# Kernel optimization log

Measured on AMD Instinct MI355X. Metric: run time of the kernel, lower is better.

The kernel has to match this reference:

```python
import jax, jax.numpy as jnp
import numpy as np

B, N, K = 4, 8192, 16
EMBED, HID, NCLS = 64, 128, 13
EPS = 1e-5


def _bn(x, g, b):
    # BatchNorm1d in training mode: stats over all points (B*N), per channel
    m = jnp.mean(x, axis=(0, 1), keepdims=True)
    v = jnp.var(x, axis=(0, 1), keepdims=True)
    return (x - m) * jax.lax.rsqrt(v + EPS) * g + b


def _knn_idx(pos, k):
    # pos: [B,N,3] -> k nearest neighbor indices per point (self excluded)
    sq = jnp.sum(pos * pos, -1)  # [B,N]
    d2 = sq[:, :, None] + sq[:, None, :] - 2.0 * jnp.einsum('bnd,bmd->bnm', pos, pos)
    n = pos.shape[1]
    d2 = d2 + jnp.eye(n, dtype=pos.dtype) * 1e10  # mask self (loop=False)
    _, idx = jax.lax.top_k(-d2, k)  # [B,N,k]
    return idx


def _pt_conv(x, pos, idx, w_lin, w_src, w_dst, pos_w, pos_b):
    # PyG PointTransformerConv: vector attention over neighbors (incl. self loop)
    Bc = x.shape[0]
    bidx = jnp.arange(Bc)[:, None, None]
    v = x @ w_lin          # value:  lin(x)
    a_src = x @ w_src      # lin_src(x)
    a_dst = x @ w_dst      # lin_dst(x)
    vj = v[bidx, idx]                      # [B,N,k1,C]
    aj = a_src[bidx, idx]                  # [B,N,k1,C]
    pj = pos[bidx, idx]                    # [B,N,k1,3]
    delta = (pos[:, :, None, :] - pj) @ pos_w + pos_b   # pos_nn(pos_i - pos_j)
    attn = jax.nn.softmax(a_dst[:, :, None, :] - aj + delta, axis=2)
    return jnp.sum(attn * (vj + delta), axis=2)  # sum aggregation


def setup_inputs() -> dict:
    key = jax.random.key(0)
    ks = jax.random.split(key, 20)

    def w(k, fan_in, fan_out):
        return (jax.random.normal(k, (fan_in, fan_out), jnp.float32) / np.sqrt(fan_in)).astype(jnp.float32)

    inp = {
        'points': jax.random.normal(ks[0], (B, N, 3), jnp.float32),
        'embed_w1': w(ks[1], 3, EMBED), 'embed_b1': jnp.zeros((EMBED,), jnp.float32),
        'bn1_g': jnp.ones((EMBED,), jnp.float32), 'bn1_b': jnp.zeros((EMBED,), jnp.float32),
        'embed_w2': w(ks[2], EMBED, EMBED), 'embed_b2': jnp.zeros((EMBED,), jnp.float32),
        'bne_g': jnp.ones((EMBED,), jnp.float32), 'bne_b': jnp.zeros((EMBED,), jnp.float32),
        'l0_lin': w(ks[3], EMBED, HID), 'l0_src': w(ks[4], EMBED, HID), 'l0_dst': w(ks[5], EMBED, HID),
        'l0_pos_w': w(ks[6], 3, HID), 'l0_pos_b': jnp.zeros((HID,), jnp.float32),
        'l0_bn_g': jnp.ones((HID,), jnp.float32), 'l0_bn_b': jnp.zeros((HID,), jnp.float32),
        'l1_lin': w(ks[7], HID, HID), 'l1_src': w(ks[8], HID, HID), 'l1_dst': w(ks[9], HID, HID),
        'l1_pos_w': w(ks[10], 3, HID), 'l1_pos_b': jnp.zeros((HID,), jnp.float32),
        'l1_bn_g': jnp.ones((HID,), jnp.float32), 'l1_bn_b': jnp.zeros((HID,), jnp.float32),
        'dec_w1': w(ks[11], HID, HID), 'dec_b1': jnp.zeros((HID,), jnp.float32),
        'dec_bn_g': jnp.ones((HID,), jnp.float32), 'dec_bn_b': jnp.zeros((HID,), jnp.float32),
        'dec_w2': w(ks[12], HID, NCLS), 'dec_b2': jnp.zeros((NCLS,), jnp.float32),
    }
    return inp


def reference(points, embed_w1, embed_b1, bn1_g, bn1_b, embed_w2, embed_b2,
              bne_g, bne_b,
              l0_lin, l0_src, l0_dst, l0_pos_w, l0_pos_b, l0_bn_g, l0_bn_b,
              l1_lin, l1_src, l1_dst, l1_pos_w, l1_pos_b, l1_bn_g, l1_bn_b,
              dec_w1, dec_b1, dec_bn_g, dec_bn_b, dec_w2, dec_b2):
    Bc, Nc, _ = points.shape
    # embedding MLP: Linear -> BN -> ReLU -> Linear, then BN -> ReLU
    h = points @ embed_w1 + embed_b1
    h = jax.nn.relu(_bn(h, bn1_g, bn1_b))
    h = h @ embed_w2 + embed_b2
    x = jax.nn.relu(_bn(h, bne_g, bne_b))
    # kNN graph (per batch), then append self loop (add_self_loops=True)
    idx = _knn_idx(points, K)
    self_idx = jnp.broadcast_to(jnp.arange(Nc)[None, :, None], (Bc, Nc, 1))
    idxf = jnp.concatenate([idx, self_idx], axis=-1)  # [B,N,K+1]
    x = jax.nn.relu(_bn(_pt_conv(x, points, idxf, l0_lin, l0_src, l0_dst, l0_pos_w, l0_pos_b), l0_bn_g, l0_bn_b))
    x = jax.nn.relu(_bn(_pt_conv(x, points, idxf, l1_lin, l1_src, l1_dst, l1_pos_w, l1_pos_b), l1_bn_g, l1_bn_b))
    # decoder MLP (dropout = identity at inference)
    h = jax.nn.relu(_bn(x @ dec_w1 + dec_b1, dec_bn_g, dec_bn_b))
    logits = h @ dec_w2 + dec_b2  # [B,N,num_classes]
    return logits
```

## Files before the change

### kernel.cpp

```cpp
#include <hip/hip_runtime.h>
#include <math.h>

#define BB 4
#define NN 8192
#define PP 32768
#define KNN 16

typedef float f32x2 __attribute__((ext_vector_type(2)));
typedef float f32x4 __attribute__((ext_vector_type(4)));

__device__ __forceinline__ f32x2 pk_mul(f32x2 a, f32x2 b) {
  f32x2 d; asm("v_pk_mul_f32 %0, %1, %2" : "=v"(d) : "v"(a), "v"(b)); return d;
}
__device__ __forceinline__ f32x2 pk_add(f32x2 a, f32x2 b) {
  f32x2 d; asm("v_pk_add_f32 %0, %1, %2" : "=v"(d) : "v"(a), "v"(b)); return d;
}

__global__ __launch_bounds__(256) void k_embed1(const float* __restrict__ pts,
    const float* __restrict__ w1, const float* __restrict__ b1, float* __restrict__ h1)
{
  int tid = threadIdx.x;
  int c = tid & 63, g = tid >> 6;
  float wx = w1[c], wy = w1[64 + c], wz = w1[128 + c], bc = b1[c];
  int base = blockIdx.x * 256;
  #pragma unroll 4
  for (int i = 0; i < 64; ++i) {
    int p = base + g + i * 4;
    float px = pts[p*3+0], py = pts[p*3+1], pz = pts[p*3+2];
    float h = fmaf(pz, wz, fmaf(py, wy, fmaf(px, wx, bc)));
    h1[(size_t)p*64 + c] = h;
  }
}

__global__ __launch_bounds__(256) void k_prep(const float* __restrict__ pts, float* __restrict__ pp)
{
  int t = blockIdx.x * 256 + threadIdx.x;
  int b = t >> 12, m = t & 4095;
  int c = m >> 4, l = m & 15;
  int jl = b * NN + c * 32 + l;
  int jh = jl + 16;
  float xl = pts[jl*3+0], yl = pts[jl*3+1], zl = pts[jl*3+2];
  float xh = pts[jh*3+0], yh = pts[jh*3+1], zh = pts[jh*3+2];
  float wl = __fadd_rn(__fadd_rn(__fmul_rn(xl,xl), __fmul_rn(yl,yl)), __fmul_rn(zl,zl));
  float wh = __fadd_rn(__fadd_rn(__fmul_rn(xh,xh), __fmul_rn(yh,yh)), __fmul_rn(zh,zh));
  float* o = pp + (size_t)t * 8;
  *(float4*)(o + 0) = make_float4(xl, xh, yl, yh);
  *(float4*)(o + 4) = make_float4(zl, zh, wl, wh);
}

template<int C>
__global__ __launch_bounds__(256) void k_stats(const float* __restrict__ src,
    float* __restrict__ gsum, float* __restrict__ gss)
{
  constexpr int GPB = 256 / C;
  int tid = threadIdx.x;
  int c = tid % C, g = tid / C;
  float s = 0.f, ss = 0.f;
  for (int p = blockIdx.x * GPB + g; p < PP; p += gridDim.x * GPB) {
    float v = src[(size_t)p*C + c];
    s += v; ss = fmaf(v, v, ss);
  }
  __shared__ float ls[256], lq[256];
  ls[tid] = s; lq[tid] = ss;
  __syncthreads();
  if (tid < C) {
    float a = 0.f, b2 = 0.f;
    #pragma unroll
    for (int i = 0; i < GPB; ++i) { a += ls[tid + i*C]; b2 += lq[tid + i*C]; }
    atomicAdd(gsum + tid, a);
    atomicAdd(gss + tid, b2);
  }
}

__global__ void k_finalize(int C, const float* __restrict__ gsum, const float* __restrict__ gss,
    const float* __restrict__ gg, const float* __restrict__ bb,
    float* __restrict__ sc, float* __restrict__ sh)
{
  int c = threadIdx.x;
  if (c >= C) return;
  float mean = gsum[c] * (1.0f / PP);
  float var  = gss[c] * (1.0f / PP) - mean * mean;
  float s = gg[c] / sqrtf(var + 1e-5f);
  sc[c] = s;
  sh[c] = bb[c] - mean * s;
}

template<int K, int COUT>
__global__ __launch_bounds__(256) void k_proj(const float* __restrict__ in,
    const float* __restrict__ sc, const float* __restrict__ sh,
    const float* __restrict__ W0, const float* __restrict__ W1, const float* __restrict__ W2,
    const float* __restrict__ B0, const float* __restrict__ B1, const float* __restrict__ B2,
    float* __restrict__ O0, float* __restrict__ O1, float* __restrict__ O2)
{
  constexpr int PTS = 64;
  constexpr int CW = 8;
  constexpr int CG = COUT / CW;
  constexpr int PW = PTS * CG / 256;
  const float* W  = (blockIdx.y == 0) ? W0 : (blockIdx.y == 1) ? W1 : W2;
  const float* Bb = (blockIdx.y == 0) ? B0 : (blockIdx.y == 1) ? B1 : B2;
  float*       O  = (blockIdx.y == 0) ? O0 : (blockIdx.y == 1) ? O1 : O2;
  __shared__ float xs[PTS][K + 1];
  int tid = threadIdx.x;
  int pbase = blockIdx.x * PTS;
  constexpr int T4 = PTS * K / 4;
  for (int i = tid; i < T4; i += 256) {
    int p = i / (K/4), k = (i % (K/4)) * 4;
    float4 v = *(const float4*)(in + (size_t)(pbase + p)*K + k);
    v.x = fmaxf(fmaf(v.x, sc[k+0], sh[k+0]), 0.f);
    v.y = fmaxf(fmaf(v.y, sc[k+1], sh[k+1]), 0.f);
    v.z = fmaxf(fmaf(v.z, sc[k+2], sh[k+2]), 0.f);
    v.w = fmaxf(fmaf(v.w, sc[k+3], sh[k+3]), 0.f);
    xs[p][k+0] = v.x; xs[p][k+1] = v.y; xs[p][k+2] = v.z; xs[p][k+3] = v.w;
  }
  __syncthreads();
  int cg = tid % CG, pg = tid / CG;
  int c0 = cg * CW, p0 = pg * PW;
  float acc[PW][CW];
  #pragma unroll
  for (int i = 0; i < PW; ++i) {
    #pragma unroll
    for (int j = 0; j < CW; ++j) acc[i][j] = 0.f;
  }
  #pragma unroll 4
  for (int k = 0; k < K; ++k) {
    float4 wa = *(const float4*)(W + (size_t)k*COUT + c0);
    float4 wb = *(const float4*)(W + (size_t)k*COUT + c0 + 4);
    #pragma unroll
    for (int i = 0; i < PW; ++i) {
      float x = xs[p0 + i][k];
      acc[i][0] = fmaf(x, wa.x, acc[i][0]);
      acc[i][1] = fmaf(x, wa.y, acc[i][1]);
      acc[i][2] = fmaf(x, wa.z, acc[i][2]);
      acc[i][3] = fmaf(x, wa.w, acc[i][3]);
      acc[i][4] = fmaf(x, wb.x, acc[i][4]);
      acc[i][5] = fmaf(x, wb.y, acc[i][5]);
      acc[i][6] = fmaf(x, wb.z, acc[i][6]);
      acc[i][7] = fmaf(x, wb.w, acc[i][7]);
    }
  }
  float bj[CW];
  #pragma unroll
  for (int j = 0; j < CW; ++j) bj[j] = Bb ? Bb[c0 + j] : 0.f;
  #pragma unroll
  for (int i = 0; i < PW; ++i) {
    float* op = O + (size_t)(pbase + p0 + i)*COUT + c0;
    *(float4*)(op)     = make_float4(acc[i][0]+bj[0], acc[i][1]+bj[1], acc[i][2]+bj[2], acc[i][3]+bj[3]);
    *(float4*)(op + 4) = make_float4(acc[i][4]+bj[4], acc[i][5]+bj[5], acc[i][6]+bj[6], acc[i][7]+bj[7]);
  }
}

__global__ __launch_bounds__(256, 8) void k_knn(const float* __restrict__ pp, int* __restrict__ idxout)
{
  int tid = threadIdx.x;
  int lane = tid & 63;
  int l16 = lane & 15;
  int g64 = lane & 48;
  int wv = (blockIdx.x * 256 + tid) >> 6;
  int b  = wv >> 11;
  int qbase = (wv * 4) & (NN - 1);
  int qc = qbase >> 5;
  int qr = (qbase & 31) + (lane >> 4);
  const float* pb = pp + (size_t)b * (NN * 4);

  float qx, qy, qz, qw;
  {
    int qslot = qc * 16 + (qr & 15);
    int qh = (qr >> 4) & 1;
    const float* qp = pb + (size_t)qslot * 8 + qh;
    qx = qp[0]; qy = qp[2]; qz = qp[4]; qw = qp[6];
  }
  f32x2 qx2; qx2.x = qx; qx2.y = qx;
  f32x2 qy2; qy2.x = qy; qy2.y = qy;
  f32x2 qz2; qz2.x = qz; qz2.y = qz;
  f32x2 qw2; qw2.x = qw; qw2.y = qw;

  int addr_push = (lane + 1) << 2;
  int addr_tau  = (g64 + 15) << 2;

  float lval = 3.4e38f;
  int   lidx = 0;
  float tau  = 3.4e38f;

  auto half_pass = [&](float d2, int jbase) {
    unsigned long long bal = __ballot(d2 < tau);
    if (bal) {
      unsigned slice = (unsigned)(bal >> g64) & 0xffffu;
      while (__ballot(slice != 0)) {
        bool live = slice != 0;
        int src = __ffs((int)slice) - 1;
        slice &= slice - 1;
        int ab = (g64 + (src & 15)) << 2;
        float v = __uint_as_float(__builtin_amdgcn_ds_bpermute(ab, __float_as_uint(d2)));
        if (!live) v = 3.4e38f;
        int jc = jbase + src;
        float pv = __uint_as_float(__builtin_amdgcn_ds_permute(addr_push, __float_as_uint(lval)));
        int   pi = __builtin_amdgcn_ds_permute(addr_push, lidx);
        bool atpos = (l16 == 0) || (pv <= v);
        if (lval > v) {
          lval = atpos ? v  : pv;
          lidx = atpos ? jc : pi;
        }
      }
      tau = __uint_as_float(__builtin_amdgcn_ds_bpermute(addr_tau, __float_as_uint(lval)));
    }
  };

  const float* cp = pb + (size_t)l16 * 8;

  {
    f32x4 A  = *(const f32x4*)(cp + 0);
    f32x4 Bq = *(const f32x4*)(cp + 4);
    cp += 128;
    f32x2 xs = __builtin_shufflevector(A, A, 0, 1);
    f32x2 ys = __builtin_shufflevector(A, A, 2, 3);
    f32x2 zs = __builtin_shufflevector(Bq, Bq, 0, 1);
    f32x2 ws = __builtin_shufflevector(Bq, Bq, 2, 3);
    f32x2 dot = pk_add(pk_add(pk_mul(qx2, xs), pk_mul(qy2, ys)), pk_mul(qz2, zs));
    f32x2 s2  = pk_add(qw2, ws);
    f32x2 t2  = pk_add(dot, dot);
    float d2lo = __fsub_rn(s2.x, t2.x);
    float d2hi = __fsub_rn(s2.y, t2.y);
    if (qc == 0) {
      bool lo = qr < 16;
      int  tl = lo ? qr : qr - 16;
      if (l16 == tl) { if (lo) d2lo = 3.4e38f; else d2hi = 3.4e38f; }
    }
    float v = d2lo; int ix = l16;
    #pragma unroll
    for (int k = 2; k <= 16; k <<= 1) {
      #pragma unroll
      for (int j = k >> 1; j >= 1; j >>= 1) {
        float ov = __shfl_xor(v, j, 16);
        int   oi = __shfl_xor(ix, j, 16);
        bool up    = (l16 & k) == 0;
        bool lower = (l16 & j) == 0;
        bool lt = (ov < v) || (ov == v && oi < ix);
        if ((up == lower) ? lt : !lt) { v = ov; ix = oi; }
      }
    }
    lval = v; lidx = ix;
    tau = __uint_as_float(__builtin_amdgcn_ds_bpermute(addr_tau, __float_as_uint(lval)));
    half_pass(d2hi, 16);
  }

  for (int c = 1; c < 256; ++c) {
    f32x4 A  = *(const f32x4*)(cp + 0);
    f32x4 Bq = *(const f32x4*)(cp + 4);
    cp += 128;
    f32x2 xs = __builtin_shufflevector(A, A, 0, 1);
    f32x2 ys = __builtin_shufflevector(A, A, 2, 3);
    f32x2 zs = __builtin_shufflevector(Bq, Bq, 0, 1);
    f32x2 ws = __builtin_shufflevector(Bq, Bq, 2, 3);
    f32x2 dot = pk_add(pk_add(pk_mul(qx2, xs), pk_mul(qy2, ys)), pk_mul(qz2, zs));
    f32x2 s2  = pk_add(qw2, ws);
    f32x2 t2  = pk_add(dot, dot);
    float d2lo = __fsub_rn(s2.x, t2.x);
    float d2hi = __fsub_rn(s2.y, t2.y);
    if (c == qc) {
      bool lo = qr < 16;
      int  tl = lo ? qr : qr - 16;
      if (l16 == tl) { if (lo) d2lo = 3.4e38f; else d2hi = 3.4e38f; }
    }
    half_pass(d2lo, c * 32);
    half_pass(d2hi, c * 32 + 16);
  }

  idxout[(size_t)wv * 64 + lane] = lidx;
}

__global__ __launch_bounds__(256) void k_conv(const float* __restrict__ V, const float* __restrict__ S,
    const float* __restrict__ D, const float* __restrict__ pts, const int* __restrict__ idx,
    const float* __restrict__ pw, const float* __restrict__ pbv, float* __restrict__ Y)
{
  int lane = threadIdx.x & 63;
  int wid  = (blockIdx.x * 256 + threadIdx.x) >> 6;
  int c0 = lane * 2;
  float2 w0  = *(const float2*)(pw + c0);
  float2 w1  = *(const float2*)(pw + 128 + c0);
  float2 w2  = *(const float2*)(pw + 256 + c0);
  float2 pb2 = *(const float2*)(pbv + c0);
  for (int p = wid; p < PP; p += 4096) {
    int b = p >> 13, self = p & (NN - 1);
    const float* pbase = pts + (size_t)b * NN * 3;
    float pix = pbase[self*3+0], piy = pbase[self*3+1], piz = pbase[self*3+2];
    float2 di = *(const float2*)(D + (size_t)p*128 + c0);
    float m0 = -3.4e38f, m1 = -3.4e38f, l0 = 0.f, l1 = 0.f, a0 = 0.f, a1 = 0.f;
    for (int t = 0; t < 17; ++t) {
      int j = (t < 16) ? idx[p*KNN + t] : self;
      float dx = pix - pbase[j*3+0];
      float dy = piy - pbase[j*3+1];
      float dz = piz - pbase[j*3+2];
      size_t off = ((size_t)b * NN + j) * 128 + c0;
      float2 sj = *(const float2*)(S + off);
      float2 vj = *(const float2*)(V + off);
      float de0 = fmaf(dz, w2.x, fmaf(dy, w1.x, fmaf(dx, w0.x, pb2.x)));
      float de1 = fmaf(dz, w2.y, fmaf(dy, w1.y, fmaf(dx, w0.y, pb2.y)));
      float g0 = di.x - sj.x + de0;
      float g1 = di.y - sj.y + de1;
      float mn0 = fmaxf(m0, g0), mn1 = fmaxf(m1, g1);
      float cr0 = __expf(m0 - mn0), cr1 = __expf(m1 - mn1);
      float e0  = __expf(g0 - mn0), e1  = __expf(g1 - mn1);
      l0 = fmaf(l0, cr0, e0);
      l1 = fmaf(l1, cr1, e1);
      a0 = fmaf(a0, cr0, e0 * (vj.x + de0));
      a1 = fmaf(a1, cr1, e1 * (vj.y + de1));
      m0 = mn0; m1 = mn1;
    }
    float2 o; o.x = a0 / l0; o.y = a1 / l1;
    *(float2*)(Y + (size_t)p*128 + c0) = o;
  }
}

__global__ __launch_bounds__(256) void k_dec2(const float* __restrict__ T,
    const float* __restrict__ sc, const float* __restrict__ sh,
    const float* __restrict__ W, const float* __restrict__ bias, float* __restrict__ out)
{
  __shared__ float xs[64][132];
  __shared__ float wt[13][128];
  int tid = threadIdx.x;
  int pb = blockIdx.x * 64;
  for (int i = tid; i < 13 * 128; i += 256) {
    int cls = i >> 7, k = i & 127;
    wt[cls][k] = W[k*13 + cls];
  }
  for (int i = tid; i < 64 * 32; i += 256) {
    int p = i >> 5, k = (i & 31) * 4;
    float4 v = *(const float4*)(T + (size_t)(pb + p)*128 + k);
    v.x = fmaxf(fmaf(v.x, sc[k+0], sh[k+0]), 0.f);
    v.y = fmaxf(fmaf(v.y, sc[k+1], sh[k+1]), 0.f);
    v.z = fmaxf(fmaf(v.z, sc[k+2], sh[k+2]), 0.f);
    v.w = fmaxf(fmaf(v.w, sc[k+3], sh[k+3]), 0.f);
    xs[p][k+0] = v.x; xs[p][k+1] = v.y; xs[p][k+2] = v.z; xs[p][k+3] = v.w;
  }
  __syncthreads();
  for (int o = tid; o < 64 * 13; o += 256) {
    int p = o / 13, cls = o - p * 13;
    float acc = bias[cls];
    const float4* xr = (const float4*)&xs[p][0];
    const float4* wr = (const float4*)&wt[cls][0];
    #pragma unroll 8
    for (int k4 = 0; k4 < 32; ++k4) {
      float4 a = xr[k4], w = wr[k4];
      acc = fmaf(a.x, w.x, acc);
      acc = fmaf(a.y, w.y, acc);
      acc = fmaf(a.z, w.z, acc);
      acc = fmaf(a.w, w.w, acc);
    }
    out[(size_t)(pb + p)*13 + cls] = acc;
  }
}

extern "C" void kernel_launch(void* const* d_in, const int* in_sizes, int n_in,
                              void* d_out, int out_size, void* d_ws, size_t ws_size,
                              hipStream_t stream)
{
  const float* pts      = (const float*)d_in[0];
  const float* embed_w1 = (const float*)d_in[1];
  const float* embed_b1 = (const float*)d_in[2];
  const float* bn1_g    = (const float*)d_in[3];
  const float* bn1_b    = (const float*)d_in[4];
  const float* embed_w2 = (const float*)d_in[5];
  const float* embed_b2 = (const float*)d_in[6];
  const float* bne_g    = (const float*)d_in[7];
  const float* bne_b    = (const float*)d_in[8];
  const float* l0_lin   = (const float*)d_in[9];
  const float* l0_src   = (const float*)d_in[10];
  const float* l0_dst   = (const float*)d_in[11];
  const float* l0_pos_w = (const float*)d_in[12];
  const float* l0_pos_b = (const float*)d_in[13];
  const float* l0_bn_g  = (const float*)d_in[14];
  const float* l0_bn_b  = (const float*)d_in[15];
  const float* l1_lin   = (const float*)d_in[16];
  const float* l1_src   = (const float*)d_in[17];
  const float* l1_dst   = (const float*)d_in[18];
  const float* l1_pos_w = (const float*)d_in[19];
  const float* l1_pos_b = (const float*)d_in[20];
  const float* l1_bn_g  = (const float*)d_in[21];
  const float* l1_bn_b  = (const float*)d_in[22];
  const float* dec_w1   = (const float*)d_in[23];
  const float* dec_b1   = (const float*)d_in[24];
  const float* dec_bn_g = (const float*)d_in[25];
  const float* dec_bn_b = (const float*)d_in[26];
  const float* dec_w2   = (const float*)d_in[27];
  const float* dec_b2   = (const float*)d_in[28];

  char* ws = (char*)d_ws;
  const size_t MB = 1024 * 1024;
  float* h1  = (float*)(ws + 0);
  float* h2  = (float*)(ws + 8*MB);
  int*   idx = (int*)  (ws + 16*MB);
  float* v0  = (float*)(ws + 18*MB);
  float* s0  = (float*)(ws + 34*MB);
  float* d0  = (float*)(ws + 50*MB);
  float* y0  = (float*)(ws + 66*MB);
  float* y1  = (float*)(ws + 82*MB);
  float* tt  = (float*)(ws + 0);
  float* pairs8 = (float*)(ws + 18*MB);
  float* st  = (float*)(ws + 98*MB);
  float *sum1=st+0,    *ss1=st+64,   *sc1=st+128,  *sh1=st+192;
  float *sum2=st+256,  *ss2=st+320,  *sc2=st+384,  *sh2=st+448;
  float *sum3=st+512,  *ss3=st+640,  *sc3=st+768,  *sh3=st+896;
  float *sum4=st+1024, *ss4=st+1152, *sc4=st+1280, *sh4=st+1408;
  float *sum5=st+1536, *ss5=st+1664, *sc5=st+1792, *sh5=st+1920;

  hipMemsetAsync(st, 0, 2048 * sizeof(float), stream);

  k_prep<<<64, 256, 0, stream>>>(pts, pairs8);
  k_knn<<<2048, 256, 0, stream>>>(pairs8, idx);

  k_embed1<<<128, 256, 0, stream>>>(pts, embed_w1, embed_b1, h1);
  k_stats<64><<<512, 256, 0, stream>>>(h1, sum1, ss1);
  k_finalize<<<1, 64, 0, stream>>>(64, sum1, ss1, bn1_g, bn1_b, sc1, sh1);
  k_proj<64,64><<<dim3(512,1), 256, 0, stream>>>(h1, sc1, sh1,
      embed_w2, embed_w2, embed_w2, embed_b2, embed_b2, embed_b2, h2, h2, h2);
  k_stats<64><<<512, 256, 0, stream>>>(h2, sum2, ss2);
  k_finalize<<<1, 64, 0, stream>>>(64, sum2, ss2, bne_g, bne_b, sc2, sh2);

  k_proj<64,128><<<dim3(512,3), 256, 0, stream>>>(h2, sc2, sh2,
      l0_lin, l0_src, l0_dst, nullptr, nullptr, nullptr, v0, s0, d0);
  k_conv<<<1024, 256, 0, stream>>>(v0, s0, d0, pts, idx, l0_pos_w, l0_pos_b, y0);
  k_stats<128><<<512, 256, 0, stream>>>(y0, sum3, ss3);
  k_finalize<<<1, 128, 0, stream>>>(128, sum3, ss3, l0_bn_g, l0_bn_b, sc3, sh3);

  k_proj<128,128><<<dim3(512,3), 256, 0, stream>>>(y0, sc3, sh3,
      l1_lin, l1_src, l1_dst, nullptr, nullptr, nullptr, v0, s0, d0);
  k_conv<<<1024, 256, 0, stream>>>(v0, s0, d0, pts, idx, l1_pos_w, l1_pos_b, y1);
  k_stats<128><<<512, 256, 0, stream>>>(y1, sum4, ss4);
  k_finalize<<<1, 128, 0, stream>>>(128, sum4, ss4, l1_bn_g, l1_bn_b, sc4, sh4);

  k_proj<128,128><<<dim3(512,1), 256, 0, stream>>>(y1, sc4, sh4,
      dec_w1, dec_w1, dec_w1, dec_b1, dec_b1, dec_b1, tt, tt, tt);
  k_stats<128><<<512, 256, 0, stream>>>(tt, sum5, ss5);
  k_finalize<<<1, 128, 0, stream>>>(128, sum5, ss5, dec_bn_g, dec_bn_b, sc5, sh5);
  k_dec2<<<512, 256, 0, stream>>>(tt, sc5, sh5, dec_w2, dec_b2, (float*)d_out);
}
```

Before: 689.7 us.

## Buffer kNN candidates in LDS and merge via bitonic sort on flush

Replaces the per-candidate serial insertion into the lane-distributed top-16 list with a pending buffer. Candidates that beat the threshold are compacted into shared memory using ballot/popcount. When the buffer would overflow, the 16 pending candidates are bitonic-sorted and merged with the current list. This amortises the serial permute-based insertion loop over batches of up to 16 hits, at the cost of extra LDS traffic and a tau that is refreshed less often.

```diff
diff --git a/kernel.cpp b/kernel.cpp
--- a/kernel.cpp
+++ b/kernel.cpp
@@ -5,6 +5,8 @@
 #define NN 8192
 #define PP 32768
 #define KNN 16
+#define KINF 3.4e38f
+#define PADIDX 0x7fffffff
 
 typedef float f32x2 __attribute__((ext_vector_type(2)));
 typedef float f32x4 __attribute__((ext_vector_type(4)));
@@ -151,10 +153,12 @@
 
 __global__ __launch_bounds__(256, 8) void k_knn(const float* __restrict__ pp, int* __restrict__ idxout)
 {
+  __shared__ uint2 buf[256];
   int tid = threadIdx.x;
   int lane = tid & 63;
   int l16 = lane & 15;
   int g64 = lane & 48;
+  uint2* wbuf = buf + (tid >> 6) * 64;
   int wv = (blockIdx.x * 256 + tid) >> 6;
   int b  = wv >> 11;
   int qbase = (wv * 4) & (NN - 1);
@@ -174,76 +178,60 @@
   f32x2 qz2; qz2.x = qz; qz2.y = qz;
   f32x2 qw2; qw2.x = qw; qw2.y = qw;
 
-  int addr_push = (lane + 1) << 2;
-  int addr_tau  = (g64 + 15) << 2;
-
-  float lval = 3.4e38f;
-  int   lidx = 0;
-  float tau  = 3.4e38f;
-
-  auto half_pass = [&](float d2, int jbase) {
-    unsigned long long bal = __ballot(d2 < tau);
-    if (bal) {
-      unsigned slice = (unsigned)(bal >> g64) & 0xffffu;
-      while (__ballot(slice != 0)) {
-        bool live = slice != 0;
-        int src = __ffs((int)slice) - 1;
-        slice &= slice - 1;
-        int ab = (g64 + (src & 15)) << 2;
-        float v = __uint_as_float(__builtin_amdgcn_ds_bpermute(ab, __float_as_uint(d2)));
-        if (!live) v = 3.4e38f;
-        int jc = jbase + src;
-        float pv = __uint_as_float(__builtin_amdgcn_ds_permute(addr_push, __float_as_uint(lval)));
-        int   pi = __builtin_amdgcn_ds_permute(addr_push, lidx);
-        bool atpos = (l16 == 0) || (pv <= v);
-        if (lval > v) {
-          lval = atpos ? v  : pv;
-          lidx = atpos ? jc : pi;
-        }
-      }
-      tau = __uint_as_float(__builtin_amdgcn_ds_bpermute(addr_tau, __float_as_uint(lval)));
-    }
-  };
-
-  const float* cp = pb + (size_t)l16 * 8;
-
-  {
-    f32x4 A  = *(const f32x4*)(cp + 0);
-    f32x4 Bq = *(const f32x4*)(cp + 4);
-    cp += 128;
-    f32x2 xs = __builtin_shufflevector(A, A, 0, 1);
-    f32x2 ys = __builtin_shufflevector(A, A, 2, 3);
-    f32x2 zs = __builtin_shufflevector(Bq, Bq, 0, 1);
-    f32x2 ws = __builtin_shufflevector(Bq, Bq, 2, 3);
-    f32x2 dot = pk_add(pk_add(pk_mul(qx2, xs), pk_mul(qy2, ys)), pk_mul(qz2, zs));
-    f32x2 s2  = pk_add(qw2, ws);
-    f32x2 t2  = pk_add(dot, dot);
-    float d2lo = __fsub_rn(s2.x, t2.x);
-    float d2hi = __fsub_rn(s2.y, t2.y);
-    if (qc == 0) {
-      bool lo = qr < 16;
-      int  tl = lo ? qr : qr - 16;
-      if (l16 == tl) { if (lo) d2lo = 3.4e38f; else d2hi = 3.4e38f; }
-    }
-    float v = d2lo; int ix = l16;
+  float lval = KINF; int lidx = PADIDX;
+  float pval = KINF; int pidx = PADIDX;
+  int   pcnt = 0;
+  float tau  = KINF;
+  unsigned lmask = (1u << l16) - 1;
+
+  auto flush = [&]() {
+    float v = (l16 >= pcnt) ? KINF : pval;
+    int  ix = (l16 >= pcnt) ? PADIDX : pidx;
     #pragma unroll
     for (int k = 2; k <= 16; k <<= 1) {
       #pragma unroll
-      for (int j = k >> 1; j >= 1; j >>= 1) {
-        float ov = __shfl_xor(v, j, 16);
-        int   oi = __shfl_xor(ix, j, 16);
-        bool up    = (l16 & k) == 0;
-        bool lower = (l16 & j) == 0;
-        bool lt = (ov < v) || (ov == v && oi < ix);
-        if ((up == lower) ? lt : !lt) { v = ov; ix = oi; }
+      for (int m = k >> 1; m >= 1; m >>= 1) {
+        float ov = __shfl_xor(v, m, 16);
+        int   oi = __shfl_xor(ix, m, 16);
+        bool dirUp = (l16 & k) == 0;
+        bool lower = (l16 & m) == 0;
+        bool oLt = (ov < v) || (ov == v && oi < ix);
+        if ((dirUp == lower) ? oLt : !oLt) { v = ov; ix = oi; }
       }
     }
-    lval = v; lidx = ix;
-    tau = __uint_as_float(__builtin_amdgcn_ds_bpermute(addr_tau, __float_as_uint(lval)));
-    half_pass(d2hi, 16);
-  }
-
-  for (int c = 1; c < 256; ++c) {
+    float rv = __shfl_xor(v, 15, 16);
+    int   ri = __shfl_xor(ix, 15, 16);
+    bool t = (rv < lval) || (rv == lval && ri < lidx);
+    float nv = t ? rv : lval;
+    int   ni = t ? ri : lidx;
+    #pragma unroll
+    for (int m = 8; m >= 1; m >>= 1) {
+      float ov = __shfl_xor(nv, m, 16);
+      int   oi = __shfl_xor(ni, m, 16);
+      bool lower = (l16 & m) == 0;
+      bool oLt = (ov < nv) || (ov == nv && oi < ni);
+      if (lower ? oLt : !oLt) { nv = ov; ni = oi; }
+    }
+    lval = nv; lidx = ni;
+    tau = __shfl(lval, 15, 16);
+    pcnt = 0;
+  };
+
+  auto append = [&](unsigned long long bal, bool hit, float d2, int j) {
+    unsigned slice = (unsigned)(bal >> g64) & 0xffffu;
+    int h   = __popc(slice);
+    int pos = __popc(slice & lmask);
+    if (__ballot(pcnt + h > 16)) flush();
+    if (hit) wbuf[g64 + pcnt + pos] = make_uint2(__float_as_uint(d2), (unsigned)j);
+    uint2 r = wbuf[lane];
+    bool targ = (l16 >= pcnt) && (l16 < pcnt + h);
+    pval = targ ? __uint_as_float(r.x) : pval;
+    pidx = targ ? (int)r.y : pidx;
+    pcnt += h;
+  };
+
+  const float* cp = pb + (size_t)l16 * 8;
+  for (int c = 0; c < 256; ++c) {
     f32x4 A  = *(const f32x4*)(cp + 0);
     f32x4 Bq = *(const f32x4*)(cp + 4);
     cp += 128;
@@ -259,11 +247,16 @@
     if (c == qc) {
       bool lo = qr < 16;
       int  tl = lo ? qr : qr - 16;
-      if (l16 == tl) { if (lo) d2lo = 3.4e38f; else d2hi = 3.4e38f; }
-    }
-    half_pass(d2lo, c * 32);
-    half_pass(d2hi, c * 32 + 16);
-  }
+      if (l16 == tl) { if (lo) d2lo = KINF; else d2hi = KINF; }
+    }
+    bool hlo = d2lo < tau;
+    unsigned long long blo = __ballot(hlo);
+    if (blo) append(blo, hlo, d2lo, c * 32 + l16);
+    bool hhi = d2hi < tau;
+    unsigned long long bhi = __ballot(hhi);
+    if (bhi) append(bhi, hhi, d2hi, c * 32 + 16 + l16);
+  }
+  flush();
 
   idxout[(size_t)wv * 64 + lane] = lidx;
 }
```

Result: no change. 698.9 us (+1.3%).

## Fuse BatchNorm statistics into producer kernels and finalize inside consumers

Applied to the files above, without the earlier changes.

Per-channel sum and sum-of-squares accumulation moves into the epilogues of embed1, proj and conv, so the separate k_stats passes no longer re-read each activation tensor. The finalize step (mean, variance, scale, shift) is now computed per block inside the consuming proj and dec2 kernels, which removes five tiny k_finalize launches. The cost is extra shuffles, shared-memory reductions and atomics in each producer, plus a few redundant rsqrt computations per block.

```diff
diff --git a/kernel.cpp b/kernel.cpp
--- a/kernel.cpp
+++ b/kernel.cpp
@@ -17,18 +17,30 @@
 }
 
 __global__ __launch_bounds__(256) void k_embed1(const float* __restrict__ pts,
-    const float* __restrict__ w1, const float* __restrict__ b1, float* __restrict__ h1)
+    const float* __restrict__ w1, const float* __restrict__ b1, float* __restrict__ h1,
+    float* __restrict__ gsum, float* __restrict__ gss)
 {
   int tid = threadIdx.x;
   int c = tid & 63, g = tid >> 6;
   float wx = w1[c], wy = w1[64 + c], wz = w1[128 + c], bc = b1[c];
   int base = blockIdx.x * 256;
+  float s = 0.f, ss = 0.f;
   #pragma unroll 4
   for (int i = 0; i < 64; ++i) {
     int p = base + g + i * 4;
     float px = pts[p*3+0], py = pts[p*3+1], pz = pts[p*3+2];
     float h = fmaf(pz, wz, fmaf(py, wy, fmaf(px, wx, bc)));
     h1[(size_t)p*64 + c] = h;
+    s += h; ss = fmaf(h, h, ss);
+  }
+  __shared__ float ls[256], lq[256];
+  ls[tid] = s; lq[tid] = ss;
+  __syncthreads();
+  if (tid < 64) {
+    float a  = ls[tid] + ls[tid+64] + ls[tid+128] + ls[tid+192];
+    float b2 = lq[tid] + lq[tid+64] + lq[tid+128] + lq[tid+192];
+    atomicAdd(gsum + tid, a);
+    atomicAdd(gss  + tid, b2);
   }
 }
 
@@ -48,49 +60,14 @@
   *(float4*)(o + 4) = make_float4(zl, zh, wl, wh);
 }
 
-template<int C>
-__global__ __launch_bounds__(256) void k_stats(const float* __restrict__ src,
-    float* __restrict__ gsum, float* __restrict__ gss)
-{
-  constexpr int GPB = 256 / C;
-  int tid = threadIdx.x;
-  int c = tid % C, g = tid / C;
-  float s = 0.f, ss = 0.f;
-  for (int p = blockIdx.x * GPB + g; p < PP; p += gridDim.x * GPB) {
-    float v = src[(size_t)p*C + c];
-    s += v; ss = fmaf(v, v, ss);
-  }
-  __shared__ float ls[256], lq[256];
-  ls[tid] = s; lq[tid] = ss;
-  __syncthreads();
-  if (tid < C) {
-    float a = 0.f, b2 = 0.f;
-    #pragma unroll
-    for (int i = 0; i < GPB; ++i) { a += ls[tid + i*C]; b2 += lq[tid + i*C]; }
-    atomicAdd(gsum + tid, a);
-    atomicAdd(gss + tid, b2);
-  }
-}
-
-__global__ void k_finalize(int C, const float* __restrict__ gsum, const float* __restrict__ gss,
-    const float* __restrict__ gg, const float* __restrict__ bb,
-    float* __restrict__ sc, float* __restrict__ sh)
-{
-  int c = threadIdx.x;
-  if (c >= C) return;
-  float mean = gsum[c] * (1.0f / PP);
-  float var  = gss[c] * (1.0f / PP) - mean * mean;
-  float s = gg[c] / sqrtf(var + 1e-5f);
-  sc[c] = s;
-  sh[c] = bb[c] - mean * s;
-}
-
-template<int K, int COUT>
+template<int K, int COUT, bool STATS>
 __global__ __launch_bounds__(256) void k_proj(const float* __restrict__ in,
-    const float* __restrict__ sc, const float* __restrict__ sh,
+    const float* __restrict__ gsumI, const float* __restrict__ gssI,
+    const float* __restrict__ gamma, const float* __restrict__ beta,
     const float* __restrict__ W0, const float* __restrict__ W1, const float* __restrict__ W2,
     const float* __restrict__ B0, const float* __restrict__ B1, const float* __restrict__ B2,
-    float* __restrict__ O0, float* __restrict__ O1, float* __restrict__ O2)
+    float* __restrict__ O0, float* __restrict__ O1, float* __restrict__ O2,
+    float* __restrict__ gsumO, float* __restrict__ gssO)
 {
   constexpr int PTS = 64;
   constexpr int CW = 8;
@@ -100,16 +77,25 @@
   const float* Bb = (blockIdx.y == 0) ? B0 : (blockIdx.y == 1) ? B1 : B2;
   float*       O  = (blockIdx.y == 0) ? O0 : (blockIdx.y == 1) ? O1 : O2;
   __shared__ float xs[PTS][K + 1];
+  __shared__ float scs[K], shs[K];
   int tid = threadIdx.x;
+  if (tid < K) {
+    float mean = gsumI[tid] * (1.0f / PP);
+    float var  = gssI[tid] * (1.0f / PP) - mean * mean;
+    float s = gamma[tid] / sqrtf(var + 1e-5f);
+    scs[tid] = s;
+    shs[tid] = beta[tid] - mean * s;
+  }
+  __syncthreads();
   int pbase = blockIdx.x * PTS;
   constexpr int T4 = PTS * K / 4;
   for (int i = tid; i < T4; i += 256) {
     int p = i / (K/4), k = (i % (K/4)) * 4;
     float4 v = *(const float4*)(in + (size_t)(pbase + p)*K + k);
-    v.x = fmaxf(fmaf(v.x, sc[k+0], sh[k+0]), 0.f);
-    v.y = fmaxf(fmaf(v.y, sc[k+1], sh[k+1]), 0.f);
-    v.z = fmaxf(fmaf(v.z, sc[k+2], sh[k+2]), 0.f);
-    v.w = fmaxf(fmaf(v.w, sc[k+3], sh[k+3]), 0.f);
+    v.x = fmaxf(fmaf(v.x, scs[k+0], shs[k+0]), 0.f);
+    v.y = fmaxf(fmaf(v.y, scs[k+1], shs[k+1]), 0.f);
+    v.z = fmaxf(fmaf(v.z, scs[k+2], shs[k+2]), 0.f);
+    v.w = fmaxf(fmaf(v.w, scs[k+3], shs[k+3]), 0.f);
     xs[p][k+0] = v.x; xs[p][k+1] = v.y; xs[p][k+2] = v.z; xs[p][k+3] = v.w;
   }
   __syncthreads();
@@ -141,11 +127,44 @@
   float bj[CW];
   #pragma unroll
   for (int j = 0; j < CW; ++j) bj[j] = Bb ? Bb[c0 + j] : 0.f;
+  float sj[CW], qj[CW];
+  #pragma unroll
+  for (int j = 0; j < CW; ++j) { sj[j] = 0.f; qj[j] = 0.f; }
   #pragma unroll
   for (int i = 0; i < PW; ++i) {
     float* op = O + (size_t)(pbase + p0 + i)*COUT + c0;
-    *(float4*)(op)     = make_float4(acc[i][0]+bj[0], acc[i][1]+bj[1], acc[i][2]+bj[2], acc[i][3]+bj[3]);
-    *(float4*)(op + 4) = make_float4(acc[i][4]+bj[4], acc[i][5]+bj[5], acc[i][6]+bj[6], acc[i][7]+bj[7]);
+    float o0 = acc[i][0]+bj[0], o1 = acc[i][1]+bj[1], o2 = acc[i][2]+bj[2], o3 = acc[i][3]+bj[3];
+    float o4 = acc[i][4]+bj[4], o5 = acc[i][5]+bj[5], o6 = acc[i][6]+bj[6], o7 = acc[i][7]+bj[7];
+    *(float4*)(op)     = make_float4(o0, o1, o2, o3);
+    *(float4*)(op + 4) = make_float4(o4, o5, o6, o7);
+    if (STATS) {
+      sj[0]+=o0; sj[1]+=o1; sj[2]+=o2; sj[3]+=o3; sj[4]+=o4; sj[5]+=o5; sj[6]+=o6; sj[7]+=o7;
+      qj[0]=fmaf(o0,o0,qj[0]); qj[1]=fmaf(o1,o1,qj[1]); qj[2]=fmaf(o2,o2,qj[2]); qj[3]=fmaf(o3,o3,qj[3]);
+      qj[4]=fmaf(o4,o4,qj[4]); qj[5]=fmaf(o5,o5,qj[5]); qj[6]=fmaf(o6,o6,qj[6]); qj[7]=fmaf(o7,o7,qj[7]);
+    }
+  }
+  if (STATS) {
+    #pragma unroll
+    for (int off = CG; off < 64; off <<= 1) {
+      #pragma unroll
+      for (int j = 0; j < CW; ++j) {
+        sj[j] += __shfl_xor(sj[j], off);
+        qj[j] += __shfl_xor(qj[j], off);
+      }
+    }
+    __shared__ float ws[4][COUT], wq[4][COUT];
+    int wid = tid >> 6, lane = tid & 63;
+    if (lane < CG) {
+      #pragma unroll
+      for (int j = 0; j < CW; ++j) { ws[wid][lane*CW+j] = sj[j]; wq[wid][lane*CW+j] = qj[j]; }
+    }
+    __syncthreads();
+    if (tid < COUT) {
+      float a  = ws[0][tid] + ws[1][tid] + ws[2][tid] + ws[3][tid];
+      float b2 = wq[0][tid] + wq[1][tid] + wq[2][tid] + wq[3][tid];
+      atomicAdd(gsumO + tid, a);
+      atomicAdd(gssO  + tid, b2);
+    }
   }
 }
 
@@ -270,15 +289,18 @@
 
 __global__ __launch_bounds__(256) void k_conv(const float* __restrict__ V, const float* __restrict__ S,
     const float* __restrict__ D, const float* __restrict__ pts, const int* __restrict__ idx,
-    const float* __restrict__ pw, const float* __restrict__ pbv, float* __restrict__ Y)
-{
-  int lane = threadIdx.x & 63;
-  int wid  = (blockIdx.x * 256 + threadIdx.x) >> 6;
+    const float* __restrict__ pw, const float* __restrict__ pbv, float* __restrict__ Y,
+    float* __restrict__ gsum, float* __restrict__ gss)
+{
+  int tid = threadIdx.x;
+  int lane = tid & 63;
+  int wid  = (blockIdx.x * 256 + tid) >> 6;
   int c0 = lane * 2;
   float2 w0  = *(const float2*)(pw + c0);
   float2 w1  = *(const float2*)(pw + 128 + c0);
   float2 w2  = *(const float2*)(pw + 256 + c0);
   float2 pb2 = *(const float2*)(pbv + c0);
+  float st0 = 0.f, st1 = 0.f, sq0 = 0.f, sq1 = 0.f;
   for (int p = wid; p < PP; p += 4096) {
     int b = p >> 13, self = p & (NN - 1);
     const float* pbase = pts + (size_t)b * NN * 3;
@@ -308,17 +330,40 @@
     }
     float2 o; o.x = a0 / l0; o.y = a1 / l1;
     *(float2*)(Y + (size_t)p*128 + c0) = o;
+    st0 += o.x; st1 += o.y;
+    sq0 = fmaf(o.x, o.x, sq0); sq1 = fmaf(o.y, o.y, sq1);
+  }
+  __shared__ float cs[4][128], cq[4][128];
+  int w = tid >> 6;
+  cs[w][c0] = st0; cs[w][c0+1] = st1;
+  cq[w][c0] = sq0; cq[w][c0+1] = sq1;
+  __syncthreads();
+  if (tid < 128) {
+    float a  = cs[0][tid] + cs[1][tid] + cs[2][tid] + cs[3][tid];
+    float b2 = cq[0][tid] + cq[1][tid] + cq[2][tid] + cq[3][tid];
+    atomicAdd(gsum + tid, a);
+    atomicAdd(gss  + tid, b2);
   }
 }
 
 __global__ __launch_bounds__(256) void k_dec2(const float* __restrict__ T,
-    const float* __restrict__ sc, const float* __restrict__ sh,
+    const float* __restrict__ gsumI, const float* __restrict__ gssI,
+    const float* __restrict__ gamma, const float* __restrict__ beta,
     const float* __restrict__ W, const float* __restrict__ bias, float* __restrict__ out)
 {
   __shared__ float xs[64][132];
   __shared__ float wt[13][128];
+  __shared__ float scs[128], shs[128];
   int tid = threadIdx.x;
   int pb = blockIdx.x * 64;
+  if (tid < 128) {
+    float mean = gsumI[tid] * (1.0f / PP);
+    float var  = gssI[tid] * (1.0f / PP) - mean * mean;
+    float s = gamma[tid] / sqrtf(var + 1e-5f);
+    scs[tid] = s;
+    shs[tid] = beta[tid] - mean * s;
+  }
+  __syncthreads();
   for (int i = tid; i < 13 * 128; i += 256) {
     int cls = i >> 7, k = i & 127;
     wt[cls][k] = W[k*13 + cls];
@@ -326,10 +371,10 @@
   for (int i = tid; i < 64 * 32; i += 256) {
     int p = i >> 5, k = (i & 31) * 4;
     float4 v = *(const float4*)(T + (size_t)(pb + p)*128 + k);
-    v.x = fmaxf(fmaf(v.x, sc[k+0], sh[k+0]), 0.f);
-    v.y = fmaxf(fmaf(v.y, sc[k+1], sh[k+1]), 0.f);
-    v.z = fmaxf(fmaf(v.z, sc[k+2], sh[k+2]), 0.f);
-    v.w = fmaxf(fmaf(v.w, sc[k+3], sh[k+3]), 0.f);
+    v.x = fmaxf(fmaf(v.x, scs[k+0], shs[k+0]), 0.f);
+    v.y = fmaxf(fmaf(v.y, scs[k+1], shs[k+1]), 0.f);
+    v.z = fmaxf(fmaf(v.z, scs[k+2], shs[k+2]), 0.f);
+    v.w = fmaxf(fmaf(v.w, scs[k+3], shs[k+3]), 0.f);
     xs[p][k+0] = v.x; xs[p][k+1] = v.y; xs[p][k+2] = v.z; xs[p][k+3] = v.w;
   }
   __syncthreads();
@@ -397,40 +442,30 @@
   float* tt  = (float*)(ws + 0);
   float* pairs8 = (float*)(ws + 18*MB);
   float* st  = (float*)(ws + 98*MB);
-  float *sum1=st+0,    *ss1=st+64,   *sc1=st+128,  *sh1=st+192;
-  float *sum2=st+256,  *ss2=st+320,  *sc2=st+384,  *sh2=st+448;
-  float *sum3=st+512,  *ss3=st+640,  *sc3=st+768,  *sh3=st+896;
-  float *sum4=st+1024, *ss4=st+1152, *sc4=st+1280, *sh4=st+1408;
-  float *sum5=st+1536, *ss5=st+1664, *sc5=st+1792, *sh5=st+1920;
+  float *sum1=st+0,    *ss1=st+64;
+  float *sum2=st+256,  *ss2=st+320;
+  float *sum3=st+512,  *ss3=st+640;
+  float *sum4=st+1024, *ss4=st+1152;
+  float *sum5=st+1536, *ss5=st+1664;
 
   hipMemsetAsync(st, 0, 2048 * sizeof(float), stream);
 
   k_prep<<<64, 256, 0, stream>>>(pts, pairs8);
   k_knn<<<2048, 256, 0, stream>>>(pairs8, idx);
 
-  k_embed1<<<128, 256, 0, stream>>>(pts, embed_w1, embed_b1, h1);
-  k_stats<64><<<512, 256, 0, stream>>>(h1, sum1, ss1);
-  k_finalize<<<1, 64, 0, stream>>>(64, sum1, ss1, bn1_g, bn1_b, sc1, sh1);
-  k_proj<64,64><<<dim3(512,1), 256, 0, stream>>>(h1, sc1, sh1,
-      embed_w2, embed_w2, embed_w2, embed_b2, embed_b2, embed_b2, h2, h2, h2);
-  k_stats<64><<<512, 256, 0, stream>>>(h2, sum2, ss2);
-  k_finalize<<<1, 64, 0, stream>>>(64, sum2, ss2, bne_g, bne_b, sc2, sh2);
-
-  k_proj<64,128><<<dim3(512,3), 256, 0, stream>>>(h2, sc2, sh2,
-      l0_lin, l0_src, l0_dst, nullptr, nullptr, nullptr, v0, s0, d0);
-  k_conv<<<1024, 256, 0, stream>>>(v0, s0, d0, pts, idx, l0_pos_w, l0_pos_b, y0);
-  k_stats<128><<<512, 256, 0, stream>>>(y0, sum3, ss3);
-  k_finalize<<<1, 128, 0, stream>>>(128, sum3, ss3, l0_bn_g, l0_bn_b, sc3, sh3);
-
-  k_proj<128,128><<<dim3(512,3), 256, 0, stream>>>(y0, sc3, sh3,
-      l1_lin, l1_src, l1_dst, nullptr, nullptr, nullptr, v0, s0, d0);
-  k_conv<<<1024, 256, 0, stream>>>(v0, s0, d0, pts, idx, l1_pos_w, l1_pos_b, y1);
-  k_stats<128><<<512, 256, 0, stream>>>(y1, sum4, ss4);
-  k_finalize<<<1, 128, 0, stream>>>(128, sum4, ss4, l1_bn_g, l1_bn_b, sc4, sh4);
-
-  k_proj<128,128><<<dim3(512,1), 256, 0, stream>>>(y1, sc4, sh4,
-      dec_w1, dec_w1, dec_w1, dec_b1, dec_b1, dec_b1, tt, tt, tt);
-  k_stats<128><<<512, 256, 0, stream>>>(tt, sum5, ss5);
-  k_finalize<<<1, 128, 0, stream>>>(128, sum5, ss5, dec_bn_g, dec_bn_b, sc5, sh5);
-  k_dec2<<<512, 256, 0, stream>>>(tt, sc5, sh5, dec_w2, dec_b2, (float*)d_out);
-}
+  k_embed1<<<128, 256, 0, stream>>>(pts, embed_w1, embed_b1, h1, sum1, ss1);
+  k_proj<64,64,true><<<dim3(512,1), 256, 0, stream>>>(h1, sum1, ss1, bn1_g, bn1_b,
+      embed_w2, embed_w2, embed_w2, embed_b2, embed_b2, embed_b2, h2, h2, h2, sum2, ss2);
+
+  k_proj<64,128,false><<<dim3(512,3), 256, 0, stream>>>(h2, sum2, ss2, bne_g, bne_b,
+      l0_lin, l0_src, l0_dst, nullptr, nullptr, nullptr, v0, s0, d0, nullptr, nullptr);
+  k_conv<<<1024, 256, 0, stream>>>(v0, s0, d0, pts, idx, l0_pos_w, l0_pos_b, y0, sum3, ss3);
+
+  k_proj<128,128,false><<<dim3(512,3), 256, 0, stream>>>(y0, sum3, ss3, l0_bn_g, l0_bn_b,
+      l1_lin, l1_src, l1_dst, nullptr, nullptr, nullptr, v0, s0, d0, nullptr, nullptr);
+  k_conv<<<1024, 256, 0, stream>>>(v0, s0, d0, pts, idx, l1_pos_w, l1_pos_b, y1, sum4, ss4);
+
+  k_proj<128,128,true><<<dim3(512,1), 256, 0, stream>>>(y1, sum4, ss4, l1_bn_g, l1_bn_b,
+      dec_w1, dec_w1, dec_w1, dec_b1, dec_b1, dec_b1, tt, tt, tt, sum5, ss5);
+  k_dec2<<<512, 256, 0, stream>>>(tt, sum5, ss5, dec_bn_g, dec_bn_b, dec_w2, dec_b2, (float*)d_out);
+}
```

After: 643.7 us. -6.7%, faster.
